# Kernel optimization log

Hardware: AMD Instinct MI355X
Metric: run time of the kernel (lower is better)

## Reference

```python
import jax, jax.numpy as jnp
import numpy as np

SENSOR_DIM = 256
MODEL_DIM = 512
NUM_DATASETS = 8


def setup_inputs() -> dict:
    key = jax.random.key(0)
    k1, k2, k3 = jax.random.split(key, 3)
    x = jax.random.normal(k1, (32, 200, 1024), dtype=jnp.float32)
    dataset_id = jax.random.randint(k2, (32,), 0, NUM_DATASETS)
    # Conv1d weight [out_ch, in_ch, k] and bias, as in torch.nn.Conv1d
    W = jax.random.normal(k3, (NUM_DATASETS * MODEL_DIM, SENSOR_DIM, 3), dtype=jnp.float32) * 0.02
    b = jnp.zeros((NUM_DATASETS * MODEL_DIM,), dtype=jnp.float32)
    return {"x": x, "dataset_id": dataset_id, "W": W, "b": b}


def reference(x, dataset_id, W, b):
    B, c_in, T = x.shape
    # DatasetPadding: zero-pad channel dim up to sensor_dim
    if c_in < SENSOR_DIM:
        x = jnp.pad(x, ((0, 0), (0, SENSOR_DIM - c_in), (0, 0)))
    # Conv1d(sensor_dim -> num_datasets*model_dim, kernel=3, padding=1)
    y = jax.lax.conv_general_dilated(
        x, W, window_strides=(1,), padding=((1, 1),),
        dimension_numbers=("NCH", "OIH", "NCH"))
    y = y + b[None, :, None]
    y = jax.nn.gelu(y, approximate=False)  # torch GELU default = exact erf
    # unflatten channels to (num_datasets, model_dim) and select per-example dataset slice
    y = y.reshape(B, NUM_DATASETS, MODEL_DIM, T)
    onehot = jax.nn.one_hot(dataset_id, NUM_DATASETS, dtype=y.dtype)  # [B, D]
    out = jnp.einsum("bdmt,bd->bmt", y, onehot)  # [B, model_dim, T]
    return out
```

## Files before the change

kernel.cpp:

```cpp
#include <hip/hip_runtime.h>


typedef unsigned short u16;
typedef __attribute__((ext_vector_type(8))) short bf16x8;
typedef __attribute__((ext_vector_type(4))) float f32x4;

#define CIN 200
#define CINP 224
#define T 1024
#define BATCH 32
#define MD 512
#define XT_ROWS 1026
#define NCHUNK 7
#define XP_PITCH 202
#define TT 256
#define XROWS (TT + 2)
#define XGRAN (XROWS * 4)
#define WGRAN 1536

__device__ __forceinline__ u16 f2bf(float f) {
    unsigned u = __float_as_uint(f);
    u += 0x7FFFu + ((u >> 16) & 1u);
    return (u16)(u >> 16);
}

__device__ __forceinline__ void g2l16(void* lds, const void* g) {
    __builtin_amdgcn_global_load_lds(
        (const __attribute__((address_space(1))) unsigned int*)(uintptr_t)g,
        (__attribute__((address_space(3))) unsigned int*)(unsigned)(uintptr_t)lds,
        16, 0, 0);
}

__global__ __launch_bounds__(256) void prep(const float* __restrict__ x,
                                            const float* __restrict__ W,
                                            u16* __restrict__ xt,
                                            u16* __restrict__ wt) {
    __shared__ u16 tile[64 * XP_PITCH];
    const int tid = threadIdx.x;
    if (blockIdx.x < 512) {
        const int b  = blockIdx.x >> 4;
        const int bx = blockIdx.x & 15;
        const int t0 = bx * 64;
        const int tl = tid & 63;
        const int w  = tid >> 6;
        const float* xb = x + (size_t)b * CIN * T + t0 + tl;
        for (int i = w; i < CIN; i += 4)
            tile[tl * XP_PITCH + i] = f2bf(xb[(size_t)i * T]);
        __syncthreads();
        u16* xrow = xt + ((size_t)b * XT_ROWS + 1 + t0) * CINP;
        for (int it = 0; it < 16; ++it) {
            int r = it * 4 + w;
            if (tl < 56) {
                ushort4 v = {0, 0, 0, 0};
                if (tl < 50) {
                    const u16* p = tile + r * XP_PITCH + tl * 4;
                    v.x = p[0]; v.y = p[1]; v.z = p[2]; v.w = p[3];
                }
                *(ushort4*)(xrow + (size_t)r * CINP + tl * 4) = v;
            }
        }
        if (bx == 0 && tid < 112)
            ((unsigned*)(xt + (size_t)b * XT_ROWS * CINP))[tid] = 0;
        if (bx == 15 && tid < 112)
            ((unsigned*)(xt + ((size_t)b * XT_ROWS + 1025) * CINP))[tid] = 0;
    } else {
        int idx = (blockIdx.x - 512) * 256 + tid;
        int o = idx / CINP;
        int i = idx - o * CINP;
        const float* wp = W + (size_t)o * 768 + i * 3;
        u16* wo = wt + (size_t)o * 3 * CINP + i;
        float w0 = wp[0], w1 = wp[1], w2 = wp[2];
        wo[0]        = f2bf(w0);
        wo[CINP]     = f2bf(w1);
        wo[2 * CINP] = f2bf(w2);
    }
}

__global__ __launch_bounds__(256, 2) void conv_mfma(const u16* __restrict__ xt,
                                                    const u16* __restrict__ wt,
                                                    const int* __restrict__ dsid,
                                                    const float* __restrict__ bias,
                                                    float* __restrict__ out) {
    __shared__ __align__(16) u16 xs[XGRAN * 8];
    __shared__ __align__(16) u16 wsm[WGRAN * 8];

    const int tid = threadIdx.x;
    const int wave = tid >> 6, lane = tid & 63;
    const int l = lane & 15, quad = lane >> 4;
    const int wm  = (wave & 1) * 64;
    const int wti = (wave >> 1) * 128;

    const int id = blockIdx.x;
    const int tb = (id >> 5) * 8 + (id & 7);
    const int m0 = ((id >> 3) & 3) * 128;
    const int t0 = (tb & 3) * TT;
    const int b  = tb >> 2;
    const int d  = dsid[b];
    const int obase = d * MD + m0;

    f32x4 acc[4][8];
#pragma unroll
    for (int mi = 0; mi < 4; ++mi)
#pragma unroll
        for (int ti = 0; ti < 8; ++ti) acc[mi][ti] = (f32x4){0.f, 0.f, 0.f, 0.f};

    const u16* xbase = xt + ((size_t)b * XT_ROWS + t0) * CINP;
    const u16* wbase = wt + (size_t)obase * 3 * CINP;

    const u16* xsrc[5]; u16* xdst[5];
#pragma unroll
    for (int k = 0; k < 5; ++k) {
        int g = tid + k * 256;
        int r = g >> 2, p = g & 3, s = p ^ ((r >> 1) & 3);
        if (g < XGRAN) { xsrc[k] = xbase + (size_t)r * CINP + s * 8; xdst[k] = xs + (size_t)(g & ~63) * 8; }
        else           { xsrc[k] = xbase;                            xdst[k] = xs; }
    }
    const u16* wsrc[6]; u16* wdst[6];
#pragma unroll
    for (int k = 0; k < 6; ++k) {
        int g = tid + k * 256;
        int p = g & 3, m = (g >> 2) & 127, kk = g >> 9;
        int s = p ^ ((m >> 1) & 3);
        wsrc[k] = wbase + ((size_t)m * 3 + kk) * CINP + s * 8;
        wdst[k] = wsm + (size_t)(g & ~63) * 8;
    }

    for (int c = 0; c < NCHUNK; ++c) {
        const int ic = c * 32;
#pragma unroll
        for (int k = 0; k < 5; ++k)
            if (tid + k * 256 < XGRAN) g2l16(xdst[k], xsrc[k] + ic);
#pragma unroll
        for (int k = 0; k < 6; ++k)
            g2l16(wdst[k], wsrc[k] + ic);
        __syncthreads();

#pragma unroll
        for (int tap = 0; tap < 3; ++tap) {
            bf16x8 a[4];
#pragma unroll
            for (int mi = 0; mi < 4; ++mi) {
                int mr = tap * 128 + wm + mi * 16 + l;
                a[mi] = *(const bf16x8*)(wsm + ((size_t)mr * 4 + (quad ^ ((mr >> 1) & 3))) * 8);
            }
#pragma unroll
            for (int ti = 0; ti < 8; ++ti) {
                int row = wti + ti * 16 + l + tap;
                bf16x8 bv = *(const bf16x8*)(xs + ((size_t)row * 4 + (quad ^ ((row >> 1) & 3))) * 8);
#pragma unroll
                for (int mi = 0; mi < 4; ++mi)
                    acc[mi][ti] = __builtin_amdgcn_mfma_f32_16x16x32_bf16(a[mi], bv, acc[mi][ti], 0, 0, 0);
            }
        }
        __syncthreads();
    }

#pragma unroll
    for (int mi = 0; mi < 4; ++mi) {
        float bv[4];
#pragma unroll
        for (int r = 0; r < 4; ++r)
            bv[r] = bias[obase + wm + mi * 16 + quad * 4 + r];
#pragma unroll
        for (int ti = 0; ti < 8; ++ti) {
            int t = t0 + wti + ti * 16 + l;
#pragma unroll
            for (int r = 0; r < 4; ++r) {
                int m = wm + mi * 16 + quad * 4 + r;
                float v = acc[mi][ti][r] + bv[r];
                float p2 = v * v;
                float z2 = v * fmaf(p2, -0.10295089f, -2.30243665f);
                float e = __builtin_amdgcn_exp2f(z2);
                float g = v * __builtin_amdgcn_rcpf(1.0f + e);
                out[((size_t)(b * MD + m0 + m)) * T + t] = g;
            }
        }
    }
}

extern "C" void kernel_launch(void* const* d_in, const int* in_sizes, int n_in,
                              void* d_out, int out_size, void* d_ws, size_t ws_size,
                              hipStream_t stream) {
    const float* x    = (const float*)d_in[0];
    const int*   dsid = (const int*)d_in[1];
    const float* W    = (const float*)d_in[2];
    const float* bias = (const float*)d_in[3];
    float* out = (float*)d_out;

    u16* xt = (u16*)d_ws;
    u16* wt = xt + (size_t)BATCH * XT_ROWS * CINP;

    prep<<<512 + 3584, 256, 0, stream>>>(x, W, xt, wt);
    conv_mfma<<<512, 256, 0, stream>>>(xt, wt, dsid, bias, out);
}
```

Measured before the change: 122.2 us.

## Double-buffer LDS chunks and halve M tile to 64 with 1024 blocks

Measured after the change: 134.1 us. 1.1x slower.

```diff
diff --git a/kernel.cpp b/kernel.cpp
--- a/kernel.cpp
+++ b/kernel.cpp
@@ -13,10 +13,11 @@
 #define XT_ROWS 1026
 #define NCHUNK 7
 #define XP_PITCH 202
+#define MW 64
 #define TT 256
 #define XROWS (TT + 2)
 #define XGRAN (XROWS * 4)
-#define WGRAN 1536
+#define WGRAN (3 * MW * 4)
 
 __device__ __forceinline__ u16 f2bf(float f) {
     unsigned u = __float_as_uint(f);
@@ -76,83 +77,96 @@
     }
 }
 
-__global__ __launch_bounds__(256, 2) void conv_mfma(const u16* __restrict__ xt,
-                                                    const u16* __restrict__ wt,
-                                                    const int* __restrict__ dsid,
-                                                    const float* __restrict__ bias,
-                                                    float* __restrict__ out) {
-    __shared__ __align__(16) u16 xs[XGRAN * 8];
-    __shared__ __align__(16) u16 wsm[WGRAN * 8];
+__global__ __launch_bounds__(256) void conv_mfma(const u16* __restrict__ xt,
+                                                 const u16* __restrict__ wt,
+                                                 const int* __restrict__ dsid,
+                                                 const float* __restrict__ bias,
+                                                 float* __restrict__ out) {
+    __shared__ __align__(16) u16 xs[2][XGRAN * 8];
+    __shared__ __align__(16) u16 wsm[2][WGRAN * 8];
 
     const int tid = threadIdx.x;
     const int wave = tid >> 6, lane = tid & 63;
     const int l = lane & 15, quad = lane >> 4;
-    const int wm  = (wave & 1) * 64;
-    const int wti = (wave >> 1) * 128;
+    const int wti = wave * 64;
 
     const int id = blockIdx.x;
-    const int tb = (id >> 5) * 8 + (id & 7);
-    const int m0 = ((id >> 3) & 3) * 128;
+    const int m0 = ((id >> 3) & 7) * MW;
+    const int tb = (id >> 6) * 8 + (id & 7);
     const int t0 = (tb & 3) * TT;
     const int b  = tb >> 2;
     const int d  = dsid[b];
     const int obase = d * MD + m0;
 
-    f32x4 acc[4][8];
+    f32x4 acc[4][4];
 #pragma unroll
     for (int mi = 0; mi < 4; ++mi)
 #pragma unroll
-        for (int ti = 0; ti < 8; ++ti) acc[mi][ti] = (f32x4){0.f, 0.f, 0.f, 0.f};
+        for (int ti = 0; ti < 4; ++ti) acc[mi][ti] = (f32x4){0.f, 0.f, 0.f, 0.f};
 
     const u16* xbase = xt + ((size_t)b * XT_ROWS + t0) * CINP;
     const u16* wbase = wt + (size_t)obase * 3 * CINP;
 
-    const u16* xsrc[5]; u16* xdst[5];
+    const u16* xsrc[5]; unsigned xdo[5];
 #pragma unroll
     for (int k = 0; k < 5; ++k) {
         int g = tid + k * 256;
         int r = g >> 2, p = g & 3, s = p ^ ((r >> 1) & 3);
-        if (g < XGRAN) { xsrc[k] = xbase + (size_t)r * CINP + s * 8; xdst[k] = xs + (size_t)(g & ~63) * 8; }
-        else           { xsrc[k] = xbase;                            xdst[k] = xs; }
-    }
-    const u16* wsrc[6]; u16* wdst[6];
-#pragma unroll
-    for (int k = 0; k < 6; ++k) {
+        if (g < XGRAN) { xsrc[k] = xbase + (size_t)r * CINP + s * 8; xdo[k] = (unsigned)(g & ~63) * 8; }
+        else           { xsrc[k] = xbase;                            xdo[k] = 0; }
+    }
+    const u16* wsrc[3]; unsigned wdo[3];
+#pragma unroll
+    for (int k = 0; k < 3; ++k) {
         int g = tid + k * 256;
-        int p = g & 3, m = (g >> 2) & 127, kk = g >> 9;
-        int s = p ^ ((m >> 1) & 3);
-        wsrc[k] = wbase + ((size_t)m * 3 + kk) * CINP + s * 8;
-        wdst[k] = wsm + (size_t)(g & ~63) * 8;
-    }
+        int p = g & 3, row = g >> 2;
+        int m = row & 63, tap = row >> 6;
+        int s = p ^ ((row >> 1) & 3);
+        wsrc[k] = wbase + ((size_t)m * 3 + tap) * CINP + s * 8;
+        wdo[k] = (unsigned)(g & ~63) * 8;
+    }
+
+#pragma unroll
+    for (int k = 0; k < 5; ++k)
+        if (tid + k * 256 < XGRAN) g2l16(&xs[0][0] + xdo[k], xsrc[k]);
+#pragma unroll
+    for (int k = 0; k < 3; ++k)
+        g2l16(&wsm[0][0] + wdo[k], wsrc[k]);
 
     for (int c = 0; c < NCHUNK; ++c) {
-        const int ic = c * 32;
-#pragma unroll
-        for (int k = 0; k < 5; ++k)
-            if (tid + k * 256 < XGRAN) g2l16(xdst[k], xsrc[k] + ic);
-#pragma unroll
-        for (int k = 0; k < 6; ++k)
-            g2l16(wdst[k], wsrc[k] + ic);
+        const int cur = c & 1;
         __syncthreads();
 
+        if (c + 1 < NCHUNK) {
+            const int ic = (c + 1) * 32;
+            const int nxt = cur ^ 1;
+#pragma unroll
+            for (int k = 0; k < 5; ++k)
+                if (tid + k * 256 < XGRAN) g2l16(&xs[nxt][0] + xdo[k], xsrc[k] + ic);
+#pragma unroll
+            for (int k = 0; k < 3; ++k)
+                g2l16(&wsm[nxt][0] + wdo[k], wsrc[k] + ic);
+        }
+
+        const u16* xb = &xs[cur][0];
+        const u16* wb = &wsm[cur][0];
 #pragma unroll
         for (int tap = 0; tap < 3; ++tap) {
             bf16x8 a[4];
 #pragma unroll
             for (int mi = 0; mi < 4; ++mi) {
-                int mr = tap * 128 + wm + mi * 16 + l;
-                a[mi] = *(const bf16x8*)(wsm + ((size_t)mr * 4 + (quad ^ ((mr >> 1) & 3))) * 8);
-            }
-#pragma unroll
-            for (int ti = 0; ti < 8; ++ti) {
+                int mr = tap * 64 + mi * 16 + l;
+                a[mi] = *(const bf16x8*)(wb + ((size_t)mr * 4 + (quad ^ ((mr >> 1) & 3))) * 8);
+            }
+#pragma unroll
+            for (int ti = 0; ti < 4; ++ti) {
                 int row = wti + ti * 16 + l + tap;
-                bf16x8 bv = *(const bf16x8*)(xs + ((size_t)row * 4 + (quad ^ ((row >> 1) & 3))) * 8);
+                bf16x8 bv = *(const bf16x8*)(xb + ((size_t)row * 4 + (quad ^ ((row >> 1) & 3))) * 8);
 #pragma unroll
                 for (int mi = 0; mi < 4; ++mi)
                     acc[mi][ti] = __builtin_amdgcn_mfma_f32_16x16x32_bf16(a[mi], bv, acc[mi][ti], 0, 0, 0);
             }
         }
-        __syncthreads();
     }
 
 #pragma unroll
@@ -160,13 +174,13 @@
         float bv[4];
 #pragma unroll
         for (int r = 0; r < 4; ++r)
-            bv[r] = bias[obase + wm + mi * 16 + quad * 4 + r];
-#pragma unroll
-        for (int ti = 0; ti < 8; ++ti) {
+            bv[r] = bias[obase + mi * 16 + quad * 4 + r];
+#pragma unroll
+        for (int ti = 0; ti < 4; ++ti) {
             int t = t0 + wti + ti * 16 + l;
 #pragma unroll
             for (int r = 0; r < 4; ++r) {
-                int m = wm + mi * 16 + quad * 4 + r;
+                int m = mi * 16 + quad * 4 + r;
                 float v = acc[mi][ti][r] + bv[r];
                 float p2 = v * v;
                 float z2 = v * fmaf(p2, -0.10295089f, -2.30243665f);
@@ -191,5 +205,5 @@
     u16* wt = xt + (size_t)BATCH * XT_ROWS * CINP;
 
     prep<<<512 + 3584, 256, 0, stream>>>(x, W, xt, wt);
-    conv_mfma<<<512, 256, 0, stream>>>(xt, wt, dsid, bias, out);
-}
+    conv_mfma<<<1024, 256, 0, stream>>>(xt, wt, dsid, bias, out);
+}
```
